# Kernel optimization log

Hardware: AMD Instinct MI355X
Metric: run time of the kernel (lower is better)

## Reference

```python
import jax, jax.numpy as jnp
import numpy as np

B, T, C = 4, 2048, 2048
H, KV, D = 16, 4, 128          # head_dim = C // H
G = H // KV                     # query heads per kv head
ROPE_BASE = 10000.0


def _rope_tables(T, D, dtype):
    inv_freq = 1.0 / (ROPE_BASE ** (jnp.arange(0, D, 2, dtype=jnp.float32) / D))
    t = jnp.arange(T, dtype=jnp.float32)
    freqs = jnp.outer(t, inv_freq)                 # [T, D/2]
    emb = jnp.concatenate([freqs, freqs], axis=-1) # [T, D]
    return jnp.cos(emb).astype(dtype), jnp.sin(emb).astype(dtype)


def _rotate_half(x):
    x1, x2 = x[..., : x.shape[-1] // 2], x[..., x.shape[-1] // 2 :]
    return jnp.concatenate([-x2, x1], axis=-1)


def setup_inputs() -> dict:
    key = jax.random.key(0)
    ks = jax.random.split(key, 5)
    s = 0.02
    return {
        "x":  jax.random.normal(ks[0], (B, T, C), dtype=jnp.float32),
        "Wq": jax.random.normal(ks[1], (C, H * D), dtype=jnp.float32) * s,
        "Wk": jax.random.normal(ks[2], (C, KV * D), dtype=jnp.float32) * s,
        "Wv": jax.random.normal(ks[3], (C, KV * D), dtype=jnp.float32) * s,
        "Wo": jax.random.normal(ks[4], (C, C), dtype=jnp.float32) * s,
    }


def reference(x, Wq, Wk, Wv, Wo):
    Bc, Tc, Cc = x.shape
    q = (x @ Wq).reshape(Bc, Tc, H, D).transpose(0, 2, 1, 3)   # [B,H,T,D]
    k = (x @ Wk).reshape(Bc, Tc, KV, D).transpose(0, 2, 1, 3)  # [B,KV,T,D]
    v = (x @ Wv).reshape(Bc, Tc, KV, D).transpose(0, 2, 1, 3)  # [B,KV,T,D]

    cos, sin = _rope_tables(Tc, D, x.dtype)                    # [T,D]
    q = q * cos + _rotate_half(q) * sin
    k = k * cos + _rotate_half(k) * sin

    # GQA: broadcast KV heads instead of materializing repeat_interleave.
    # repeat_interleave over head dim == view q as [B,KV,G,T,D] sharing kv head.
    qg = q.reshape(Bc, KV, G, Tc, D)
    scale = D ** -0.5
    scores = jnp.einsum("bkgtd,bksd->bkgts", qg, k) * scale    # [B,KV,G,T,T]
    causal = jnp.tril(jnp.ones((Tc, Tc), dtype=bool))
    scores = jnp.where(causal, scores, jnp.finfo(scores.dtype).min)
    att = jax.nn.softmax(scores, axis=-1)
    out = jnp.einsum("bkgts,bksd->bkgtd", att, v)              # [B,KV,G,T,D]
    out = out.reshape(Bc, H, Tc, D).transpose(0, 2, 1, 3).reshape(Bc, Tc, Cc)
    return out @ Wo
```

## Files before the change

kernel.cpp:

```cpp
#include <hip/hip_runtime.h>
#include <cstdint>

#define DEV __device__ __forceinline__

typedef __attribute__((ext_vector_type(4))) float f32x4;
typedef __attribute__((ext_vector_type(4))) float float4v;
typedef __attribute__((ext_vector_type(8))) short bf16x8;
typedef __attribute__((ext_vector_type(4))) unsigned short ushort4v;
typedef __attribute__((ext_vector_type(2))) unsigned int uint2v;
typedef unsigned short u16;

static constexpr int Bb = 4, Tt = 2048, Hh = 16, KVh = 4, Dd = 128;
static constexpr int NQKV = 3072;

DEV u16 f2bf(float x) {
    union { float f; unsigned u; } v; v.f = x;
    unsigned r = v.u + 0x7FFF + ((v.u >> 16) & 1);
    return (u16)(r >> 16);
}
DEV float bf2f(u16 b) {
    union { unsigned u; float f; } v; v.u = ((unsigned)b) << 16;
    return v.f;
}
DEV unsigned cvtpk(float lo, float hi) {
    unsigned d;
    asm("v_cvt_pk_bf16_f32 %0, %1, %2" : "=v"(d) : "v"(lo), "v"(hi));
    return d;
}

typedef const void __attribute__((address_space(1)))* gas1;
typedef void __attribute__((address_space(3)))* las3;
DEV void gload16(const void* g, void* l) {
    __builtin_amdgcn_global_load_lds((gas1)g, (las3)l, 16, 0, 0);
}

__global__ __launch_bounds__(256) void cast_k(const float* __restrict__ x, u16* __restrict__ xb, long n4) {
    long id = (long)blockIdx.x * 256 + threadIdx.x;
    if (id >= n4) return;
    float4v v = *(const float4v*)&x[id * 4];
    ushort4v o;
    o[0] = f2bf(v[0]); o[1] = f2bf(v[1]); o[2] = f2bf(v[2]); o[3] = f2bf(v[3]);
    *(ushort4v*)&xb[id * 4] = o;
}

__global__ __launch_bounds__(256) void twt_k(const float* __restrict__ W, u16* __restrict__ Wt, int K, int N) {
    __shared__ float tile[32][33];
    int tx = threadIdx.x, ty = threadIdx.y;
    long n0 = (long)blockIdx.x * 32, k0 = (long)blockIdx.y * 32;
#pragma unroll
    for (int j = 0; j < 4; j++)
        tile[ty + j * 8][tx] = W[(k0 + ty + j * 8) * (long)N + n0 + tx];
    __syncthreads();
#pragma unroll
    for (int j = 0; j < 4; j++)
        Wt[(n0 + ty + j * 8) * (long)K + k0 + tx] = f2bf(tile[tx][ty + j * 8]);
}

__global__ __launch_bounds__(256) void tv_k(const u16* __restrict__ qkv, u16* __restrict__ vt) {
    __shared__ u16 tile[32][33];
    int tx = threadIdx.x, ty = threadIdx.y;
    int d0 = blockIdx.x * 32;
    int t0 = blockIdx.y * 32;
    int bk = blockIdx.z;
    int b = bk >> 2, kv = bk & 3;
#pragma unroll
    for (int j = 0; j < 4; j++)
        tile[ty + j * 8][tx] = qkv[(long)(b * Tt + t0 + ty + j * 8) * NQKV + 2560 + kv * Dd + d0 + tx];
    __syncthreads();
#pragma unroll
    for (int j = 0; j < 4; j++)
        vt[((long)(b * KVh + kv) * Dd + d0 + ty + j * 8) * Tt + t0 + tx] = tile[tx][ty + j * 8];
}

__global__ __launch_bounds__(256) void tables_k(float* __restrict__ cosb, float* __restrict__ sinb) {
    int id = blockIdx.x * 256 + threadIdx.x;
    int t = id >> 6, i = id & 63;
    float inv = powf(10000.0f, -(float)i * (1.0f / 64.0f));
    float f = (float)t * inv;
    cosb[id] = cosf(f);
    sinb[id] = sinf(f);
}

__global__ __launch_bounds__(256) void rope_k(u16* __restrict__ p, const float* __restrict__ cosb,
                                              const float* __restrict__ sinb, int nh, float scale, int total,
                                              long rowstride, int colbase) {
    int id = blockIdx.x * 256 + threadIdx.x;
    if (id >= total) return;
    int i = id & 63;
    int bth = id >> 6;
    int row = bth / nh;
    int t = row % Tt;
    u16* ptr = p + (long)row * rowstride + colbase + (bth % nh) * Dd;
    float x1 = bf2f(ptr[i]), x2 = bf2f(ptr[i + 64]);
    float c = cosb[t * 64 + i], s = sinb[t * 64 + i];
    ptr[i] = f2bf((x1 * c - x2 * s) * scale);
    ptr[i + 64] = f2bf((x2 * c + x1 * s) * scale);
}

template <int F32OUT>
__global__ __launch_bounds__(512) void gemm_k(const u16* __restrict__ A, const u16* __restrict__ Bt,
                                              void* __restrict__ Cout, int M, int N, int K) {
    __shared__ u16 lds[3][24576];
    const int tid = threadIdx.x;
    const int lane = tid & 63;
    const int w = __builtin_amdgcn_readfirstlane(tid >> 6);
    const int wm = w >> 1, wn = w & 1;
    const long m0 = (long)blockIdx.x * 256;
    const long n0 = (long)blockIdx.y * 128;
    const int NT = K >> 6;
    const int l8 = lane >> 3, s8 = lane & 7;
    const int fr = lane & 15, kg = lane >> 4;

    auto stage = [&](int t) {
        u16* base = lds[t % 3];
        const long ko = (long)t * 64;
#pragma unroll
        for (int c4 = 0; c4 < 4; c4++) {
            int c = w * 4 + c4;
            int row = c * 8 + l8;
            int slog = s8 ^ (l8 & 7);
            gload16(A + (m0 + row) * (long)K + ko + slog * 8, base + c * 512);
        }
#pragma unroll
        for (int c2 = 0; c2 < 2; c2++) {
            int c = w * 2 + c2;
            int row = c * 8 + l8;
            int slog = s8 ^ (l8 & 7);
            gload16(Bt + (n0 + row) * (long)K + ko + slog * 8, base + 16384 + c * 512);
        }
    };

    f32x4 acc[4][4] = {};
    stage(0);
    if (NT > 1) {
        stage(1);
        asm volatile("s_waitcnt vmcnt(6)" ::: "memory");
    } else {
        asm volatile("s_waitcnt vmcnt(0)" ::: "memory");
    }
    __builtin_amdgcn_s_barrier();

    for (int t = 0; t < NT; ++t) {
        if (t + 2 < NT) stage(t + 2);
        const u16* sa = lds[t % 3];
        const u16* sb = sa + 16384;
#pragma unroll
        for (int ks = 0; ks < 2; ks++) {
            bf16x8 af[4], bfr[4];
#pragma unroll
            for (int i = 0; i < 4; i++) {
                const int row = wm * 64 + i * 16 + fr;
                af[i] = *(const bf16x8*)&sa[row * 64 + (((ks * 4 + kg) ^ (row & 7)) * 8)];
                const int col = wn * 64 + i * 16 + fr;
                bfr[i] = *(const bf16x8*)&sb[col * 64 + (((ks * 4 + kg) ^ (col & 7)) * 8)];
            }
            __builtin_amdgcn_s_setprio(1);
#pragma unroll
            for (int i = 0; i < 4; i++)
#pragma unroll
                for (int j = 0; j < 4; j++)
                    acc[i][j] = __builtin_amdgcn_mfma_f32_16x16x32_bf16(af[i], bfr[j], acc[i][j], 0, 0, 0);
            __builtin_amdgcn_s_setprio(0);
        }
        if (t + 2 < NT)
            asm volatile("s_waitcnt vmcnt(6)" ::: "memory");
        else if (t + 1 < NT)
            asm volatile("s_waitcnt vmcnt(0)" ::: "memory");
        __builtin_amdgcn_s_barrier();
    }

    const int orow = (lane >> 4) * 4, ocol = lane & 15;
#pragma unroll
    for (int i = 0; i < 4; i++)
#pragma unroll
        for (int j = 0; j < 4; j++) {
            long r = m0 + wm * 64 + i * 16 + orow;
            long c = n0 + wn * 64 + j * 16 + ocol;
#pragma unroll
            for (int t = 0; t < 4; t++) {
                if (F32OUT)
                    ((float*)Cout)[(r + t) * N + c] = acc[i][j][t];
                else
                    ((u16*)Cout)[(r + t) * N + c] = f2bf(acc[i][j][t]);
            }
        }
}

__global__ __launch_bounds__(256, 2) void attn_k(const u16* __restrict__ qkv,
                                                 const u16* __restrict__ vt, u16* __restrict__ o) {
    __shared__ u16 kl[2][2][4096];
    __shared__ u16 vl[2][2][4096];
    __shared__ u16 pT[4][16][36];
    const int tid = threadIdx.x;
    const int lane = tid & 63;
    const int w = tid >> 6;
    const int kv = blockIdx.y, b = blockIdx.z;
    const int h = kv * 4 + w;
    const int fr = lane & 15, kg = lane >> 4;
    const long HD = (long)Hh * Dd;
    const long QS = (long)NQKV;
    const long kbase = (long)b * Tt * QS + 2048 + (long)kv * Dd;
    const long vbase = ((long)(b * KVh + kv)) * (long)Dd * Tt;

    auto stage = [&](int bb, int it) {
        const int s0 = it * 64;
        const int lh = lane >> 4;
#pragma unroll
        for (int s = 0; s < 2; s++) {
#pragma unroll
            for (int j = 0; j < 2; j++) {
                int c = j * 4 + w;
                int row = c * 4 + lh;
                int c16 = (lane & 15) ^ (row & 7);
                gload16(qkv + kbase + (long)(s0 + s * 32 + row) * QS + c16 * 8, &kl[bb][s][c * 512]);
            }
#pragma unroll
            for (int j = 0; j < 2; j++) {
                int c = j * 4 + w;
                int rowp = c * 4 + lh;
                int c16u = (lane & 15) ^ (rowp & 7);
                int r = rowp * 4 + (c16u >> 2);
                gload16(vt + vbase + (long)r * Tt + s0 + s * 32 + (c16u & 3) * 8, &vl[bb][s][c * 512]);
            }
        }
    };

    for (int pass = 0; pass < 2; ++pass) {
        const int qt = pass ? (int)blockIdx.x : 63 - (int)blockIdx.x;
        const int q0 = qt * 32;
        const long qbase = (long)(b * Tt + q0) * QS + (long)h * Dd;
        const long obase = (long)(b * Tt + q0) * HD + (long)h * Dd;

        bf16x8 qa[2][4];
#pragma unroll
        for (int qi = 0; qi < 2; qi++)
#pragma unroll
            for (int kc = 0; kc < 4; kc++)
                qa[qi][kc] = *(const bf16x8*)&qkv[qbase + (long)(qi * 16 + fr) * QS + kc * 32 + kg * 8];

        f32x4 ot[8][2] = {};
        float mr0 = -1e30f, mr1 = -1e30f, lr0 = 0.0f, lr1 = 0.0f;
        const int nt = (qt + 2) >> 1;

        stage(0, 0);
        __syncthreads();
        int cur = 0;
        for (int it = 0; it < nt; ++it) {
            if (it + 1 < nt) stage(cur ^ 1, it + 1);
            const int s0 = it * 64;
            f32x4 st[4][2] = {};
            __builtin_amdgcn_s_setprio(1);
#pragma unroll
            for (int kf = 0; kf < 4; kf++) {
                const int s = kf >> 1;
                const int rr = (kf & 1) * 16 + fr;
                bf16x8 ka[4];
#pragma unroll
                for (int kc = 0; kc < 4; kc++)
                    ka[kc] = *(const bf16x8*)&kl[cur][s][rr * 128 + (((kc * 4 + kg) ^ (rr & 7)) * 8)];
#pragma unroll
                for (int kc = 0; kc < 4; kc++) {
                    st[kf][0] = __builtin_amdgcn_mfma_f32_16x16x32_bf16(ka[kc], qa[0][kc], st[kf][0], 0, 0, 0);
                    st[kf][1] = __builtin_amdgcn_mfma_f32_16x16x32_bf16(ka[kc], qa[1][kc], st[kf][1], 0, 0, 0);
                }
            }
            __builtin_amdgcn_s_setprio(0);
            if (it == nt - 1) {
#pragma unroll
                for (int kf = 0; kf < 4; kf++)
#pragma unroll
                    for (int qi = 0; qi < 2; qi++) {
                        const int qq = q0 + qi * 16 + fr;
                        const int kb0 = s0 + kf * 16 + kg * 4;
#pragma unroll
                        for (int r = 0; r < 4; r++)
                            if (kb0 + r > qq) st[kf][qi][r] = -1e30f;
                    }
            }
            float tm0 = st[0][0][0], tm1 = st[0][1][0];
#pragma unroll
            for (int kf = 0; kf < 4; kf++)
#pragma unroll
                for (int r = 0; r < 4; r++)
                    if (kf | r) {
                        tm0 = fmaxf(tm0, st[kf][0][r]);
                        tm1 = fmaxf(tm1, st[kf][1][r]);
                    }
            tm0 = fmaxf(tm0, __shfl_xor(tm0, 16)); tm0 = fmaxf(tm0, __shfl_xor(tm0, 32));
            tm1 = fmaxf(tm1, __shfl_xor(tm1, 16)); tm1 = fmaxf(tm1, __shfl_xor(tm1, 32));
            if (__any(fmaxf(tm0 - mr0, tm1 - mr1) > 8.0f)) {
                float mn0 = fmaxf(mr0, tm0), mn1 = fmaxf(mr1, tm1);
                float al0 = __builtin_amdgcn_exp2f(mr0 - mn0);
                float al1 = __builtin_amdgcn_exp2f(mr1 - mn1);
                mr0 = mn0; mr1 = mn1;
                lr0 *= al0; lr1 *= al1;
#pragma unroll
                for (int df = 0; df < 8; df++) { ot[df][0] *= al0; ot[df][1] *= al1; }
            }
            float rs0 = 0.0f, rs1 = 0.0f;
#pragma unroll
            for (int kf = 0; kf < 4; kf++)
#pragma unroll
                for (int r = 0; r < 4; r++) {
                    st[kf][0][r] = __builtin_amdgcn_exp2f(st[kf][0][r] - mr0); rs0 += st[kf][0][r];
                    st[kf][1][r] = __builtin_amdgcn_exp2f(st[kf][1][r] - mr1); rs1 += st[kf][1][r];
                }
            rs0 += __shfl_xor(rs0, 16); rs0 += __shfl_xor(rs0, 32);
            rs1 += __shfl_xor(rs1, 16); rs1 += __shfl_xor(rs1, 32);
            lr0 += rs0; lr1 += rs1;
#pragma unroll
            for (int qi = 0; qi < 2; qi++)
#pragma unroll
                for (int s = 0; s < 2; s++) {
                    uint2v w0;
                    w0[0] = cvtpk(st[2 * s][qi][0], st[2 * s][qi][1]);
                    w0[1] = cvtpk(st[2 * s][qi][2], st[2 * s][qi][3]);
                    *(uint2v*)&pT[w][fr][kg * 4] = w0;
                    uint2v w1;
                    w1[0] = cvtpk(st[2 * s + 1][qi][0], st[2 * s + 1][qi][1]);
                    w1[1] = cvtpk(st[2 * s + 1][qi][2], st[2 * s + 1][qi][3]);
                    *(uint2v*)&pT[w][fr][16 + kg * 4] = w1;
                    bf16x8 bq = *(const bf16x8*)&pT[w][fr][kg * 8];
                    __builtin_amdgcn_s_setprio(1);
#pragma unroll
                    for (int df = 0; df < 8; df++) {
                        const int r = df * 16 + fr;
                        const int rowp = r >> 2;
                        const int c16 = (((r & 3) * 4 + kg) ^ (rowp & 7));
                        bf16x8 va = *(const bf16x8*)&vl[cur][s][rowp * 128 + c16 * 8];
                        ot[df][qi] = __builtin_amdgcn_mfma_f32_16x16x32_bf16(va, bq, ot[df][qi], 0, 0, 0);
                    }
                    __builtin_amdgcn_s_setprio(0);
                }
            __syncthreads();
            cur ^= 1;
        }
        const float il0 = 1.0f / lr0, il1 = 1.0f / lr1;
#pragma unroll
        for (int df = 0; df < 8; df++) {
            uint2v w0, w1;
            w0[0] = cvtpk(ot[df][0][0] * il0, ot[df][0][1] * il0);
            w0[1] = cvtpk(ot[df][0][2] * il0, ot[df][0][3] * il0);
            w1[0] = cvtpk(ot[df][1][0] * il1, ot[df][1][1] * il1);
            w1[1] = cvtpk(ot[df][1][2] * il1, ot[df][1][3] * il1);
            *(uint2v*)&o[obase + (long)(fr) * HD + df * 16 + kg * 4] = w0;
            *(uint2v*)&o[obase + (long)(16 + fr) * HD + df * 16 + kg * 4] = w1;
        }
    }
}

extern "C" void kernel_launch(void* const* d_in, const int* in_sizes, int n_in,
                              void* d_out, int out_size, void* d_ws, size_t ws_size,
                              hipStream_t stream) {
    (void)in_sizes; (void)n_in; (void)out_size; (void)ws_size;
    const float* x = (const float*)d_in[0];
    const float* Wq = (const float*)d_in[1];
    const float* Wk = (const float*)d_in[2];
    const float* Wv = (const float*)d_in[3];
    const float* Wo = (const float*)d_in[4];

    char* ws = (char*)d_ws;
    u16* xb   = (u16*)(ws + 0);
    u16* vtb  = (u16*)(ws + 50331648);
    u16* wqt  = (u16*)(ws + 58720256);
    u16* wkt  = (u16*)(ws + 67108864);
    u16* wvt  = (u16*)(ws + 69206016);
    u16* wot  = (u16*)(ws + 71303168);
    float* cosb = (float*)(ws + 79691776);
    float* sinb = (float*)(ws + 80216064);
    u16* qkv = (u16*)d_out;

    dim3 tb(32, 8);
    cast_k<<<16384, 256, 0, stream>>>(x, xb, 4194304);
    twt_k<<<dim3(64, 64), tb, 0, stream>>>(Wq, wqt, 2048, 2048);
    twt_k<<<dim3(16, 64), tb, 0, stream>>>(Wk, wkt, 2048, 512);
    twt_k<<<dim3(16, 64), tb, 0, stream>>>(Wv, wvt, 2048, 512);
    twt_k<<<dim3(64, 64), tb, 0, stream>>>(Wo, wot, 2048, 2048);
    tables_k<<<512, 256, 0, stream>>>(cosb, sinb);

    gemm_k<0><<<dim3(32, 24), 512, 0, stream>>>(xb, wqt, qkv, 8192, NQKV, 2048);

    rope_k<<<32768, 256, 0, stream>>>(qkv, cosb, sinb, 16, 0.1275174316f, 8388608, NQKV, 0);
    rope_k<<<8192, 256, 0, stream>>>(qkv, cosb, sinb, 4, 1.0f, 2097152, NQKV, 2048);
    tv_k<<<dim3(4, 64, 16), tb, 0, stream>>>(qkv, vtb);

    attn_k<<<dim3(32, 4, 4), 256, 0, stream>>>(qkv, vtb, xb);

    gemm_k<1><<<dim3(32, 16), 512, 0, stream>>>(xb, wot, d_out, 8192, 2048, 2048);
}
```

Measured before the change: 364.8 us.

## Split GEMM prefetch into A/B halves interleaved with MFMA sub-steps; remap attention grid

The GEMM main loop is unrolled into two k-substeps, and the next tile's global loads are split between them: the A-tile prefetch is issued in the first substep and the B-tile prefetch in the second. Extra barriers are added around each MFMA block. The aim is to spread memory traffic more evenly across the compute, at the cost of more barriers per iteration. The attention launch is also remapped so that blockIdx.x enumerates (batch, kv head) pairs, which changes the block scheduling order so that blocks sharing K/V may land close together in time.

```diff
diff --git a/kernel.cpp b/kernel.cpp
--- a/kernel.cpp
+++ b/kernel.cpp
@@ -111,7 +111,7 @@
     const int l8 = lane >> 3, s8 = lane & 7;
     const int fr = lane & 15, kg = lane >> 4;
 
-    auto stage = [&](int t) {
+    auto stageA = [&](int t) {
         u16* base = lds[t % 3];
         const long ko = (long)t * 64;
 #pragma unroll
@@ -121,6 +121,10 @@
             int slog = s8 ^ (l8 & 7);
             gload16(A + (m0 + row) * (long)K + ko + slog * 8, base + c * 512);
         }
+    };
+    auto stageB = [&](int t) {
+        u16* base = lds[t % 3];
+        const long ko = (long)t * 64;
 #pragma unroll
         for (int c2 = 0; c2 < 2; c2++) {
             int c = w * 2 + c2;
@@ -131,9 +135,9 @@
     };
 
     f32x4 acc[4][4] = {};
-    stage(0);
+    stageA(0); stageB(0);
     if (NT > 1) {
-        stage(1);
+        stageA(1); stageB(1);
         asm volatile("s_waitcnt vmcnt(6)" ::: "memory");
     } else {
         asm volatile("s_waitcnt vmcnt(0)" ::: "memory");
@@ -141,19 +145,19 @@
     __builtin_amdgcn_s_barrier();
 
     for (int t = 0; t < NT; ++t) {
-        if (t + 2 < NT) stage(t + 2);
         const u16* sa = lds[t % 3];
         const u16* sb = sa + 16384;
-#pragma unroll
-        for (int ks = 0; ks < 2; ks++) {
+        {
             bf16x8 af[4], bfr[4];
 #pragma unroll
             for (int i = 0; i < 4; i++) {
                 const int row = wm * 64 + i * 16 + fr;
-                af[i] = *(const bf16x8*)&sa[row * 64 + (((ks * 4 + kg) ^ (row & 7)) * 8)];
+                af[i] = *(const bf16x8*)&sa[row * 64 + ((kg ^ (row & 7)) * 8)];
                 const int col = wn * 64 + i * 16 + fr;
-                bfr[i] = *(const bf16x8*)&sb[col * 64 + (((ks * 4 + kg) ^ (col & 7)) * 8)];
-            }
+                bfr[i] = *(const bf16x8*)&sb[col * 64 + ((kg ^ (col & 7)) * 8)];
+            }
+            if (t + 2 < NT) stageA(t + 2);
+            __builtin_amdgcn_s_barrier();
             __builtin_amdgcn_s_setprio(1);
 #pragma unroll
             for (int i = 0; i < 4; i++)
@@ -161,12 +165,32 @@
                 for (int j = 0; j < 4; j++)
                     acc[i][j] = __builtin_amdgcn_mfma_f32_16x16x32_bf16(af[i], bfr[j], acc[i][j], 0, 0, 0);
             __builtin_amdgcn_s_setprio(0);
-        }
-        if (t + 2 < NT)
-            asm volatile("s_waitcnt vmcnt(6)" ::: "memory");
-        else if (t + 1 < NT)
-            asm volatile("s_waitcnt vmcnt(0)" ::: "memory");
-        __builtin_amdgcn_s_barrier();
+            __builtin_amdgcn_s_barrier();
+        }
+        {
+            bf16x8 af[4], bfr[4];
+#pragma unroll
+            for (int i = 0; i < 4; i++) {
+                const int row = wm * 64 + i * 16 + fr;
+                af[i] = *(const bf16x8*)&sa[row * 64 + (((4 + kg) ^ (row & 7)) * 8)];
+                const int col = wn * 64 + i * 16 + fr;
+                bfr[i] = *(const bf16x8*)&sb[col * 64 + (((4 + kg) ^ (col & 7)) * 8)];
+            }
+            if (t + 2 < NT) stageB(t + 2);
+            if (t + 2 < NT)
+                asm volatile("s_waitcnt vmcnt(6)" ::: "memory");
+            else if (t + 1 < NT)
+                asm volatile("s_waitcnt vmcnt(0)" ::: "memory");
+            __builtin_amdgcn_s_barrier();
+            __builtin_amdgcn_s_setprio(1);
+#pragma unroll
+            for (int i = 0; i < 4; i++)
+#pragma unroll
+                for (int j = 0; j < 4; j++)
+                    acc[i][j] = __builtin_amdgcn_mfma_f32_16x16x32_bf16(af[i], bfr[j], acc[i][j], 0, 0, 0);
+            __builtin_amdgcn_s_setprio(0);
+            __builtin_amdgcn_s_barrier();
+        }
     }
 
     const int orow = (lane >> 4) * 4, ocol = lane & 15;
@@ -194,7 +218,9 @@
     const int tid = threadIdx.x;
     const int lane = tid & 63;
     const int w = tid >> 6;
-    const int kv = blockIdx.y, b = blockIdx.z;
+    const int kvb = blockIdx.x;
+    const int kv = kvb & 3, b = kvb >> 2;
+    const int bid = blockIdx.y;
     const int h = kv * 4 + w;
     const int fr = lane & 15, kg = lane >> 4;
     const long HD = (long)Hh * Dd;
@@ -226,7 +252,7 @@
     };
 
     for (int pass = 0; pass < 2; ++pass) {
-        const int qt = pass ? (int)blockIdx.x : 63 - (int)blockIdx.x;
+        const int qt = pass ? bid : 63 - bid;
         const int q0 = qt * 32;
         const long qbase = (long)(b * Tt + q0) * QS + (long)h * Dd;
         const long obase = (long)(b * Tt + q0) * HD + (long)h * Dd;
@@ -384,7 +410,7 @@
     rope_k<<<8192, 256, 0, stream>>>(qkv, cosb, sinb, 4, 1.0f, 2097152, NQKV, 2048);
     tv_k<<<dim3(4, 64, 16), tb, 0, stream>>>(qkv, vtb);
 
-    attn_k<<<dim3(32, 4, 4), 256, 0, stream>>>(qkv, vtb, xb);
+    attn_k<<<dim3(16, 32), 256, 0, stream>>>(qkv, vtb, xb);
 
     gemm_k<1><<<dim3(32, 16), 512, 0, stream>>>(xb, wot, d_out, 8192, 2048, 2048);
 }
```

Result: faster. 351.5 us (-3.6%).
